# Kernel tuning notes

Hardware: AMD Instinct MI355X
Metric: run time of the kernel (lower is better)

Reference implementation:

```python
import jax, jax.numpy as jnp
import numpy as np

N, E, G = 100000, 3200000, 5000
EPS = 1e-5
HEADS, HC = 8, 16


def setup_inputs() -> dict:
    key = jax.random.key(0)
    k = jax.random.split(key, 12)

    def lin(kk, fi, fo):
        return (jax.random.normal(kk, (fi, fo), jnp.float32) / np.sqrt(fi)).astype(jnp.float32)

    return {
        "x": jax.random.normal(k[0], (N, 20), jnp.float32),
        "edge_index": jax.random.randint(k[1], (2, E), 0, N, dtype=jnp.int32),
        "batch": jnp.sort(jax.random.randint(k[2], (N,), 0, G, dtype=jnp.int32)),
        "W1": lin(k[3], 20, 64), "b1": jnp.zeros((64,), jnp.float32),
        "g1": jnp.ones((64,), jnp.float32), "be1": jnp.zeros((64,), jnp.float32),
        "W2": lin(k[4], 64, 32), "b2": jnp.zeros((32,), jnp.float32),
        "g2": jnp.ones((32,), jnp.float32), "be2": jnp.zeros((32,), jnp.float32),
        "W3": lin(k[5], 32, 16), "b3": jnp.zeros((16,), jnp.float32),
        "g3": jnp.ones((16,), jnp.float32), "be3": jnp.zeros((16,), jnp.float32),
        "Wg": lin(k[6], 16, HEADS * HC),
        "att_src": jax.random.normal(k[7], (HEADS, HC), jnp.float32) * 0.1,
        "att_dst": jax.random.normal(k[8], (HEADS, HC), jnp.float32) * 0.1,
        "bg": jnp.zeros((HC,), jnp.float32),
        "Wf": lin(k[9], 16, 3), "bf": jnp.zeros((3,), jnp.float32),
    }


def reference(x, edge_index, batch,
              W1, b1, g1, be1, W2, b2, g2, be2, W3, b3, g3, be3,
              Wg, att_src, att_dst, bg, Wf, bf):
    src, dst = edge_index[0], edge_index[1]
    loop = jnp.arange(N, dtype=src.dtype)
    src_sl = jnp.concatenate([src, loop])  # self-loops (GCN + GAT add_self_loops)
    dst_sl = jnp.concatenate([dst, loop])

    # GCN symmetric normalization D^-1/2 (A+I) D^-1/2
    deg = jax.ops.segment_sum(jnp.ones_like(src_sl, dtype=jnp.float32), dst_sl, N)
    dinv = jnp.where(deg > 0, 1.0 / jnp.sqrt(deg), 0.0)
    norm = (dinv[src_sl] * dinv[dst_sl])[:, None]  # [E+N, 1]

    def gcn(h, W, b):
        h = h @ W
        return jax.ops.segment_sum(h[src_sl] * norm, dst_sl, N) + b

    def bn_relu(h, g, b):  # BatchNorm1d (train-mode batch stats) + ReLU
        mu = h.mean(0)
        var = ((h - mu) ** 2).mean(0)
        return jax.nn.relu(g * (h - mu) * jax.lax.rsqrt(var + EPS) + b)

    h = bn_relu(gcn(x, W1, b1), g1, be1)   # dropout = identity (eval)
    h = bn_relu(gcn(h, W2, b2), g2, be2)
    h = bn_relu(gcn(h, W3, b3), g3, be3)

    # GATConv: heads=8, concat=False (mean over heads), eval -> no dropout
    xg = (h @ Wg).reshape(N, HEADS, HC)
    a_src = (xg * att_src).sum(-1)  # [N, H]
    a_dst = (xg * att_dst).sum(-1)
    logit = jax.nn.leaky_relu(a_src[src_sl] + a_dst[dst_sl], 0.2)  # [E+N, H]
    m = jax.ops.segment_max(logit, dst_sl, N)          # segment softmax over dst
    e = jnp.exp(logit - m[dst_sl])
    s = jax.ops.segment_sum(e, dst_sl, N)
    alpha = e / s[dst_sl]
    agg = jax.ops.segment_sum(xg[src_sl] * alpha[:, :, None], dst_sl, N)  # [N,H,C]
    hg = agg.mean(1) + bg  # [N, 16]

    pooled = jax.ops.segment_sum(hg, batch, G)  # global_add_pool -> [G, 16]
    return pooled @ Wf + bf  # [G, 3]
```

## Files before the change

kernel.cpp:

```cpp
#include <hip/hip_runtime.h>
#include <hip/hip_fp16.h>

constexpr int NN = 100000;
constexpr int EE = 3200000;
constexpr int GG = 5000;
constexpr float BNEPS = 1e-5f;

constexpr int BINS = 128;
constexpr int NPB = (NN + BINS - 1) / BINS;
constexpr int BCHUNK = 8192;
constexpr int NBCH = (EE + BCHUNK - 1) / BCHUNK;
constexpr int BINCAP2 = 96;
constexpr int BINREG = 27648;
constexpr int LCAP = 26624;
constexpr int CTR_STRIDE = 32;

typedef int int4v __attribute__((ext_vector_type(4)));


__global__ __launch_bounds__(1024) void bin_edges(const int* __restrict__ ei,
                                                  uint2* __restrict__ pairs,
                                                  int* __restrict__ binCur) {
    __shared__ int bcnt[BINS];
    __shared__ int bbase[BINS];
    __shared__ uint2 buf[BINS][BINCAP2];
    const int t = threadIdx.x;
    const int lane = t & 63, wv = t >> 6;
    for (int ch = blockIdx.x; ch < NBCH; ch += gridDim.x) {
        for (int k = t; k < BINS; k += 1024) bcnt[k] = 0;
        __syncthreads();
        const int qbase = ch * (BCHUNK / 4);
#pragma unroll
        for (int rep = 0; rep < 2; ++rep) {
            const int q = qbase + rep * 1024 + t;
            if (q < EE / 4) {
                int4v d = __builtin_nontemporal_load((const int4v*)(ei + EE) + q);
                int4v s = __builtin_nontemporal_load((const int4v*)ei + q);
                int dd[4] = {d.x, d.y, d.z, d.w};
                int ss[4] = {s.x, s.y, s.z, s.w};
#pragma unroll
                for (int k = 0; k < 4; ++k) {
                    int o = dd[k] / NPB;
                    int p = atomicAdd(&bcnt[o], 1);
                    if (p < BINCAP2) {
                        buf[o][p] = make_uint2((unsigned)dd[k], (unsigned)ss[k]);
                    } else {
                        int gp = atomicAdd(&binCur[o * CTR_STRIDE], 1);
                        pairs[(size_t)o * BINREG + gp] =
                            make_uint2((unsigned)dd[k], (unsigned)ss[k]);
                    }
                }
            }
        }
        __syncthreads();
        if (t < BINS) {
            int c = bcnt[t] < BINCAP2 ? bcnt[t] : BINCAP2;
            bbase[t] = atomicAdd(&binCur[t * CTR_STRIDE], c);
            bcnt[t] = c;
        }
        __syncthreads();
        for (int o = wv; o < BINS; o += 16) {
            const int c = bcnt[o];
            const size_t base = (size_t)o * BINREG + bbase[o];
            for (int k = lane; k < c; k += 64) pairs[base + k] = buf[o][k];
        }
        __syncthreads();
    }
}


__global__ void bin_base(const int* __restrict__ binCur, int* __restrict__ binBase) {
    __shared__ int s[BINS];
    const int t = threadIdx.x;
    const int v = binCur[t * CTR_STRIDE];
    s[t] = v;
    __syncthreads();
    for (int off = 1; off < BINS; off <<= 1) {
        int add = (t >= off) ? s[t - off] : 0;
        __syncthreads();
        s[t] += add;
        __syncthreads();
    }
    binBase[t] = s[t] - v;
}


__global__ __launch_bounds__(1024) void scatter_lds(const uint2* __restrict__ pairs,
                                                    const int* __restrict__ binCur,
                                                    const int* __restrict__ binBase,
                                                    int* __restrict__ rowptr,
                                                    float* __restrict__ dinv,
                                                    int* __restrict__ colA) {
    __shared__ int scnt[NPB];
    __shared__ int sscan[1024];
    __shared__ int lbuf[LCAP];
    const int b = blockIdx.x;
    const int t = threadIdx.x;
    const int lo = b * NPB;
    const int hi = (lo + NPB < NN) ? lo + NPB : NN;
    const int nb = hi - lo;
    const int tot = binCur[b * CTR_STRIDE];
    const int base = binBase[b];
    const uint2* p = pairs + (size_t)b * BINREG;
    for (int k = t; k < nb; k += 1024) scnt[k] = 0;
    __syncthreads();
    for (int q = t; q < tot; q += 1024) atomicAdd(&scnt[p[q].x - lo], 1);
    __syncthreads();
    const int myc = (t < nb) ? scnt[t] : 0;
    sscan[t] = myc;
    __syncthreads();
    for (int off = 1; off < 1024; off <<= 1) {
        int add = (t >= off) ? sscan[t - off] : 0;
        __syncthreads();
        sscan[t] += add;
        __syncthreads();
    }
    const int excl = sscan[t] - myc;
    if (t < nb) {
        rowptr[lo + t] = base + excl;
        dinv[lo + t] = rsqrtf((float)(myc + 1));
        scnt[t] = excl;
    }
    if (b == BINS - 1 && t == 0) rowptr[NN] = base + tot;
    __syncthreads();
    for (int q = t; q < tot; q += 1024) {
        uint2 e = p[q];
        int pos = atomicAdd(&scnt[e.x - lo], 1);
        if (pos < LCAP) lbuf[pos] = (int)e.y;
        else colA[base + pos] = (int)e.y;
    }
    __syncthreads();
    const int m = tot < LCAP ? tot : LCAP;
    for (int k = t; k < m; k += 1024) colA[base + k] = lbuf[k];
}


__global__ void scale_x(const float* __restrict__ x, const float* __restrict__ dinv,
                        __half* __restrict__ xsc) {
    int idx = blockIdx.x * blockDim.x + threadIdx.x;
    if (idx < NN * 20) {
        int n = idx / 20;
        xsc[idx] = __float2half(x[idx] * dinv[n]);
    }
}


template <int FIN, int FOUT, bool AFFINE, bool SCALED, bool STATS>
__global__ void gemm_k(const float* __restrict__ hin,
                       const float* __restrict__ sumsIn, const float* __restrict__ ssqIn,
                       const float* __restrict__ g, const float* __restrict__ be,
                       const float* __restrict__ W, const float* __restrict__ dinv,
                       const float* __restrict__ bias,
                       float* __restrict__ outF, __half* __restrict__ outH,
                       float* __restrict__ sumsOut, float* __restrict__ ssqOut) {
    constexpr int NB = 256 / FOUT;
    __shared__ float Wl[FIN * FOUT];
    __shared__ float rows[NB][FIN];
    __shared__ float aa[AFFINE ? FIN : 1], bb[AFFINE ? FIN : 1];
    const int t = threadIdx.x;
    if constexpr (AFFINE) {
        if (t < FIN) {
            float mu = sumsIn[t] / (float)NN;
            float var = ssqIn[t] / (float)NN - mu * mu;
            float a = g[t] * rsqrtf(var + BNEPS);
            aa[t] = a;
            bb[t] = be[t] - mu * a;
        }
    }
    for (int i = t; i < FIN * FOUT; i += 256) Wl[i] = W[i];
    const int c = t % FOUT, s = t / FOUT;
    const int ngrp = (NN + NB - 1) / NB;
    float sAcc = 0.f, qAcc = 0.f;
    for (int grp = blockIdx.x; grp < ngrp; grp += gridDim.x) {
        __syncthreads();
        for (int i = t; i < NB * FIN; i += 256) {
            int sn = i / FIN, k = i % FIN;
            int n2 = grp * NB + sn;
            float v = 0.f;
            if (n2 < NN) {
                v = hin[(size_t)n2 * FIN + k];
                if constexpr (AFFINE) {
                    v = aa[k] * v + bb[k];
                    v = v > 0.f ? v : 0.f;
                }
            }
            rows[sn][k] = v;
        }
        __syncthreads();
        int node = grp * NB + s;
        if (node < NN) {
            float acc = 0.f;
#pragma unroll
            for (int k = 0; k < FIN; ++k) acc += rows[s][k] * Wl[k * FOUT + c];
            if constexpr (SCALED) {
                outH[(size_t)node * FOUT + c] = __float2half(acc * dinv[node]);
            } else {
                float val = acc + bias[c];
                outF[(size_t)node * FOUT + c] = val;
                if constexpr (STATS) { sAcc += val; qAcc += val * val; }
            }
        }
    }
    if constexpr (STATS) {
        __shared__ float ls[FOUT], lq[FOUT];
        __syncthreads();
        if (t < FOUT) { ls[t] = 0.f; lq[t] = 0.f; }
        __syncthreads();
        atomicAdd(&ls[c], sAcc);
        atomicAdd(&lq[c], qAcc);
        __syncthreads();
        if (t < FOUT) { atomicAdd(&sumsOut[t], ls[t]); atomicAdd(&ssqOut[t], lq[t]); }
    }
}


template <int H2, int OUTF, bool STATS>
__global__ void agg_half(const __half2* __restrict__ src, const int* __restrict__ rowptr,
                         const int* __restrict__ colA, const float* __restrict__ dinv,
                         const float* __restrict__ bias, float* __restrict__ out,
                         float* __restrict__ sumsOut, float* __restrict__ ssqOut) {
    constexpr int SUB = 64 / H2;
    const int lane = threadIdx.x & 63;
    const int wid = (blockIdx.x * blockDim.x + threadIdx.x) >> 6;
    const int totalWaves = (gridDim.x * blockDim.x) >> 6;
    const int f = lane % H2;
    const int sub = lane / H2;
    const int stride = totalWaves * SUB;
    float bx = 0.f, by = 0.f;
    if (bias != nullptr) {
        bx = bias[2 * f];
        by = (2 * f + 1 < OUTF) ? bias[2 * f + 1] : 0.f;
    }
    const int i0 = (sub < SUB) ? wid * SUB + sub : NN;
    float sx = 0.f, qx = 0.f, sy = 0.f, qy = 0.f;
    for (int i = i0; i < NN; i += stride) {
        const int r0 = rowptr[i], r1 = rowptr[i + 1];
        float2 acc = __half22float2(src[(size_t)i * H2 + f]);
        float2 acc2 = {0.f, 0.f};
        int e = r0;
        for (; e + 3 < r1; e += 4) {
            int j0 = colA[e], j1 = colA[e + 1], j2 = colA[e + 2], j3 = colA[e + 3];
            float2 v0 = __half22float2(src[(size_t)j0 * H2 + f]);
            float2 v1 = __half22float2(src[(size_t)j1 * H2 + f]);
            float2 v2 = __half22float2(src[(size_t)j2 * H2 + f]);
            float2 v3 = __half22float2(src[(size_t)j3 * H2 + f]);
            acc.x += v0.x + v1.x;
            acc.y += v0.y + v1.y;
            acc2.x += v2.x + v3.x;
            acc2.y += v2.y + v3.y;
        }
        for (; e < r1; ++e) {
            float2 v = __half22float2(src[(size_t)colA[e] * H2 + f]);
            acc.x += v.x; acc.y += v.y;
        }
        acc.x += acc2.x; acc.y += acc2.y;
        const float d = dinv[i];
        float vx = d * acc.x + bx;
        out[(size_t)i * OUTF + 2 * f] = vx;
        if constexpr (STATS) { sx += vx; qx += vx * vx; }
        if (2 * f + 1 < OUTF) {
            float vy = d * acc.y + by;
            out[(size_t)i * OUTF + 2 * f + 1] = vy;
            if constexpr (STATS) { sy += vy; qy += vy * vy; }
        }
    }
    if constexpr (STATS) {
        __shared__ float ls[OUTF], lq[OUTF];
        const int t = threadIdx.x;
        if (t < OUTF) { ls[t] = 0.f; lq[t] = 0.f; }
        __syncthreads();
        atomicAdd(&ls[2 * f], sx);
        atomicAdd(&lq[2 * f], qx);
        if (2 * f + 1 < OUTF) {
            atomicAdd(&ls[2 * f + 1], sy);
            atomicAdd(&lq[2 * f + 1], qy);
        }
        __syncthreads();
        if (t < OUTF) { atomicAdd(&sumsOut[t], ls[t]); atomicAdd(&ssqOut[t], lq[t]); }
    }
}


__global__ void gat_mats(const float* __restrict__ Wg, const float* __restrict__ att_src,
                         const float* __restrict__ att_dst, const float* __restrict__ Wf,
                         const float* __restrict__ bg, float* __restrict__ Psrc,
                         float* __restrict__ Pdst, float* __restrict__ M,
                         float* __restrict__ bgW) {
    int t = threadIdx.x;
    if (t < 128) {
        int k = t >> 3, h = t & 7;
        float s = 0.f, d = 0.f;
        for (int c = 0; c < 16; ++c) {
            float wv = Wg[k * 128 + h * 16 + c];
            s += wv * att_src[h * 16 + c];
            d += wv * att_dst[h * 16 + c];
        }
        Psrc[k * 8 + h] = s;
        Pdst[k * 8 + h] = d;
    } else if (t < 512) {
        int m = t - 128;
        if (m < 384) {
            int hk = m / 3, j = m - hk * 3;
            int H = hk >> 4, k = hk & 15;
            float s = 0.f;
            for (int c = 0; c < 16; ++c) s += Wg[k * 128 + H * 16 + c] * Wf[c * 3 + j];
            M[hk * 3 + j] = 0.125f * s;
        }
    } else if (t < 515) {
        int j = t - 512;
        float s = 0.f;
        for (int c = 0; c < 16; ++c) s += bg[c] * Wf[c * 3 + j];
        bgW[j] = s;
    }
}


__global__ void gat_pre2(const float* __restrict__ h3,
                         const float* __restrict__ sums3, const float* __restrict__ ssq3,
                         const float* __restrict__ g3, const float* __restrict__ be3,
                         const float* __restrict__ Psrc, const float* __restrict__ Pdst,
                         float4* __restrict__ zas, float* __restrict__ adst) {
    __shared__ float Ps[128], Pd[128], aa[16], bb[16];
    int t = threadIdx.x;
    if (t < 128) { Ps[t] = Psrc[t]; Pd[t] = Pdst[t]; }
    if (t < 16) {
        float mu = sums3[t] / (float)NN;
        float var = ssq3[t] / (float)NN - mu * mu;
        float a = g3[t] * rsqrtf(var + BNEPS);
        aa[t] = a;
        bb[t] = be3[t] - mu * a;
    }
    __syncthreads();
    int n = blockIdx.x * blockDim.x + t;
    if (n >= NN) return;
    float zv[16];
#pragma unroll
    for (int k = 0; k < 16; ++k) {
        float v = h3[(size_t)n * 16 + k];
        v = aa[k] * v + bb[k];
        zv[k] = v > 0.f ? v : 0.f;
    }
    __half2 zh[8];
#pragma unroll
    for (int k = 0; k < 8; ++k) zh[k] = __floats2half2_rn(zv[2 * k], zv[2 * k + 1]);
    float as[8], ad[8];
#pragma unroll
    for (int h = 0; h < 8; ++h) { as[h] = 0.f; ad[h] = 0.f; }
#pragma unroll
    for (int k = 0; k < 16; ++k) {
        float zk = zv[k];
#pragma unroll
        for (int h = 0; h < 8; ++h) {
            as[h] += zk * Ps[k * 8 + h];
            ad[h] += zk * Pd[k * 8 + h];
        }
    }
    float4* zrow = zas + (size_t)n * 4;
    zrow[0] = ((float4*)zh)[0];
    zrow[1] = ((float4*)zh)[1];
    zrow[2] = make_float4(as[0], as[1], as[2], as[3]);
    zrow[3] = make_float4(as[4], as[5], as[6], as[7]);
    float4* d4 = (float4*)(adst + (size_t)n * 8);
    d4[0] = make_float4(ad[0], ad[1], ad[2], ad[3]);
    d4[1] = make_float4(ad[4], ad[5], ad[6], ad[7]);
}


__device__ __forceinline__ float leaky02(float x) { return x > 0.f ? x : 0.2f * x; }

__global__ void gat_agg7(const float4* __restrict__ zas, const float* __restrict__ adst,
                         const int* __restrict__ rowptr, const int* __restrict__ colA,
                         const int* __restrict__ batch, const float* __restrict__ Mg,
                         float* __restrict__ out) {
    __shared__ float Ml[384];
    for (int k = threadIdx.x; k < 384; k += 256) Ml[k] = Mg[k];
    __syncthreads();
    const int lane = threadIdx.x & 63;
    const int ls = lane & 7;
    const int q = ls & 3;
    const int hh = ls >> 2;
    const int grp = lane >> 3;
    const int gb = lane & 56;
    const int wid = (blockIdx.x * blockDim.x + threadIdx.x) >> 6;
    const int totalWaves = (gridDim.x * blockDim.x) >> 6;
    const int stride = totalWaves * 8;
    const char* zb = (const char*)zas;
    for (int i = wid * 8 + grp; i < NN; i += stride) {
        const int r0 = rowptr[i], r1 = rowptr[i + 1];
        const float adv = __builtin_nontemporal_load(adst + (size_t)i * 8 + ls);
        float acc[4][4];
        float wsum[4];
#pragma unroll
        for (int h = 0; h < 4; ++h) {
            wsum[h] = 0.f;
#pragma unroll
            for (int k = 0; k < 4; ++k) acc[h][k] = 0.f;
        }
        auto compute = [&](float av, float2 zr, bool val) {
            const __half2* zp = (const __half2*)&zr;
            const float2 f0 = __half22float2(zp[0]), f1 = __half22float2(zp[1]);
            const float zf[4] = {f0.x, f0.y, f1.x, f1.y};
            const float w = val ? __expf(leaky02(av + adv)) : 0.f;
            float wq[4];
#pragma unroll
            for (int h = 0; h < 4; ++h) wq[h] = __shfl(w, gb + hh * 4 + h);
#pragma unroll
            for (int h = 0; h < 4; ++h) {
                wsum[h] += wq[h];
#pragma unroll
                for (int k = 0; k < 4; ++k) acc[h][k] += wq[h] * zf[k];
            }
        };
        int e = r0;
        int jA = i, jB = i;
        bool vB = false;
        if (e < r1) { jB = colA[e]; ++e; vB = true; }
        const char* rowA = zb + (size_t)jA * 64;
        const char* rowB = zb + (size_t)jB * 64;
        float avA = *(const float*)(rowA + 32 + ls * 4);
        float2 zA = *(const float2*)(rowA + q * 8);
        float avB = *(const float*)(rowB + 32 + ls * 4);
        float2 zB = *(const float2*)(rowB + q * 8);
        while (true) {
            int jA2 = i, jB2 = i;
            bool vA2 = false, vB2 = false;
            if (e < r1) { jA2 = colA[e]; ++e; vA2 = true; }
            if (e < r1) { jB2 = colA[e]; ++e; vB2 = true; }
            const char* rA2 = zb + (size_t)jA2 * 64;
            const char* rB2 = zb + (size_t)jB2 * 64;
            float avA2 = *(const float*)(rA2 + 32 + ls * 4);
            float2 zA2 = *(const float2*)(rA2 + q * 8);
            float avB2 = *(const float*)(rB2 + 32 + ls * 4);
            float2 zB2 = *(const float2*)(rB2 + q * 8);
            compute(avA, zA, true);
            compute(avB, zB, vB);
            if (!vA2) break;
            avA = avA2; zA = zA2; avB = avB2; zB = zB2; vB = vB2;
        }
        float o0 = 0.f, o1 = 0.f, o2 = 0.f;
#pragma unroll
        for (int h = 0; h < 4; ++h) {
            const float inv = 1.f / wsum[h];
            const int hk0 = (hh * 4 + h) * 16 + q * 4;
#pragma unroll
            for (int k = 0; k < 4; ++k) {
                const float v = acc[h][k] * inv;
                const float* m = &Ml[(hk0 + k) * 3];
                o0 += v * m[0];
                o1 += v * m[1];
                o2 += v * m[2];
            }
        }
#pragma unroll
        for (int off = 1; off < 8; off <<= 1) {
            o0 += __shfl_xor(o0, off);
            o1 += __shfl_xor(o1, off);
            o2 += __shfl_xor(o2, off);
        }
        const int g = batch[i];
        if (ls < 3) {
            const float ov = (ls == 0) ? o0 : (ls == 1) ? o1 : o2;
            atomicAdd(&out[g * 3 + ls], ov);
        }
    }
}


__global__ void graph_bounds(const int* __restrict__ batch, int* __restrict__ gstart) {
    int n = blockIdx.x * blockDim.x + threadIdx.x;
    if (n < NN) {
        int bn = batch[n];
        int bp = (n == 0) ? -1 : batch[n - 1];
        for (int g = bp + 1; g <= bn; ++g) gstart[g] = n;
        if (n == NN - 1)
            for (int g = bn + 1; g <= GG; ++g) gstart[g] = NN;
    }
}


__global__ void pool_init(const int* __restrict__ gstart, const float* __restrict__ bgW,
                          const float* __restrict__ bf, float* __restrict__ out) {
    int g = blockIdx.x * blockDim.x + threadIdx.x;
    if (g < GG) {
        float cnt = (float)(gstart[g + 1] - gstart[g]);
#pragma unroll
        for (int j = 0; j < 3; ++j) out[g * 3 + j] = cnt * bgW[j] + bf[j];
    }
}


extern "C" void kernel_launch(void* const* d_in, const int* in_sizes, int n_in,
                              void* d_out, int out_size, void* d_ws, size_t ws_size,
                              hipStream_t stream) {
    const float* x = (const float*)d_in[0];
    const int* ei = (const int*)d_in[1];
    const int* batch = (const int*)d_in[2];
    const float* W1 = (const float*)d_in[3];  const float* b1 = (const float*)d_in[4];
    const float* g1 = (const float*)d_in[5];  const float* be1 = (const float*)d_in[6];
    const float* W2 = (const float*)d_in[7];  const float* b2 = (const float*)d_in[8];
    const float* g2 = (const float*)d_in[9];  const float* be2 = (const float*)d_in[10];
    const float* W3 = (const float*)d_in[11]; const float* b3 = (const float*)d_in[12];
    const float* g3 = (const float*)d_in[13]; const float* be3 = (const float*)d_in[14];
    const float* Wg = (const float*)d_in[15];
    const float* att_src = (const float*)d_in[16];
    const float* att_dst = (const float*)d_in[17];
    const float* bg = (const float*)d_in[18];
    const float* Wf = (const float*)d_in[19];
    const float* bf = (const float*)d_in[20];
    float* out = (float*)d_out;

    char* w = (char*)d_ws;
    auto alloc = [&](size_t bytes) -> char* {
        char* p = w;
        w += (bytes + 255) & ~(size_t)255;
        return p;
    };
    int* binCur = (int*)alloc((size_t)BINS * CTR_STRIDE * 4);
    float* sums1 = (float*)alloc(64 * 4); float* ssq1 = (float*)alloc(64 * 4);
    float* sums2 = (float*)alloc(32 * 4); float* ssq2 = (float*)alloc(32 * 4);
    float* sums3 = (float*)alloc(16 * 4); float* ssq3 = (float*)alloc(16 * 4);
    size_t zeroBytes = (size_t)(w - (char*)d_ws);
    int* binBase = (int*)alloc((size_t)BINS * 4);
    float* Psrc = (float*)alloc(128 * 4);
    float* Pdst = (float*)alloc(128 * 4);
    float* Mm = (float*)alloc(384 * 4);
    float* bgW = (float*)alloc(3 * 4);
    int* gstart = (int*)alloc((size_t)(GG + 1) * 4);
    int* rowptr = (int*)alloc((size_t)(NN + 1) * 4);
    int* colA = (int*)alloc((size_t)EE * 4);
    float* dinv = (float*)alloc((size_t)NN * 4);
    char* A = alloc((size_t)NN * 64 * 4);
    char* B = alloc((size_t)NN * 64 * 4);

    uint2*  pairs = (uint2*)A;
    __half* xsc  = (__half*)B;
    float*  aggx = (float*)(B + (size_t)NN * 32 * 2);
    float*  h1   = (float*)A;
    __half* hs2  = (__half*)B;
    float*  h2   = (float*)(B + (size_t)NN * 32 * 2);
    __half* hs3  = (__half*)A;
    float*  h3   = (float*)(A + (size_t)NN * 16 * 2);
    char*   zas  = A + (size_t)NN * 96;
    float*  adst = (float*)(A + (size_t)NN * 160);

    hipMemsetAsync(d_ws, 0, zeroBytes, stream);

    bin_edges<<<256, 1024, 0, stream>>>(ei, pairs, binCur);
    bin_base<<<1, BINS, 0, stream>>>(binCur, binBase);
    scatter_lds<<<BINS, 1024, 0, stream>>>(pairs, binCur, binBase, rowptr, dinv, colA);
    gat_mats<<<1, 1024, 0, stream>>>(Wg, att_src, att_dst, Wf, bg, Psrc, Pdst, Mm, bgW);
    graph_bounds<<<(NN + 255) / 256, 256, 0, stream>>>(batch, gstart);
    pool_init<<<(GG + 255) / 256, 256, 0, stream>>>(gstart, bgW, bf, out);

    scale_x<<<(NN * 20 + 255) / 256, 256, 0, stream>>>(x, dinv, xsc);
    agg_half<10, 20, false><<<2048, 256, 0, stream>>>((const __half2*)xsc, rowptr, colA, dinv,
                                                      nullptr, aggx, nullptr, nullptr);
    gemm_k<20, 64, false, false, true><<<2048, 256, 0, stream>>>(
        aggx, nullptr, nullptr, nullptr, nullptr, W1, dinv, b1, h1, nullptr, sums1, ssq1);

    gemm_k<64, 32, true, true, false><<<2048, 256, 0, stream>>>(
        h1, sums1, ssq1, g1, be1, W2, dinv, nullptr, nullptr, hs2, nullptr, nullptr);
    agg_half<16, 32, true><<<2048, 256, 0, stream>>>((const __half2*)hs2, rowptr, colA, dinv,
                                                     b2, h2, sums2, ssq2);

    gemm_k<32, 16, true, true, false><<<2048, 256, 0, stream>>>(
        h2, sums2, ssq2, g2, be2, W3, dinv, nullptr, nullptr, hs3, nullptr, nullptr);
    agg_half<8, 16, true><<<2048, 256, 0, stream>>>((const __half2*)hs3, rowptr, colA, dinv,
                                                    b3, h3, sums3, ssq3);

    gat_pre2<<<(NN + 255) / 256, 256, 0, stream>>>(h3, sums3, ssq3, g3, be3, Psrc, Pdst,
                                                   (float4*)zas, adst);
    gat_agg7<<<3200, 256, 0, stream>>>((const float4*)zas, adst, rowptr, colA, batch, Mm, out);
}
```

Before: 468.9 us.

## Pack edge pairs into 32-bit words, store intermediates in fp16, split layer-2 aggregation

Edge binning now packs each edge's local destination offset and source index into one 32-bit word instead of a uint2, halving the traffic through the pairs buffer. All intermediate activations (aggx, h1, h2, h3) are stored as fp16 instead of fp32, cutting the bytes each layer reads and writes. The 32-wide layer-2 aggregation is split into two 16-wide feature halves with separate buffers, and the next GEMM reads both halves. The risks are lower precision in the pre-BatchNorm activations, although the statistics are still accumulated in fp32, and an extra pass over the CSR graph for layer 2.

```diff
diff --git a/kernel.cpp b/kernel.cpp
--- a/kernel.cpp
+++ b/kernel.cpp
@@ -18,12 +18,13 @@
 typedef int int4v __attribute__((ext_vector_type(4)));
 
 
+
 __global__ __launch_bounds__(1024) void bin_edges(const int* __restrict__ ei,
-                                                  uint2* __restrict__ pairs,
+                                                  unsigned* __restrict__ pairs,
                                                   int* __restrict__ binCur) {
     __shared__ int bcnt[BINS];
     __shared__ int bbase[BINS];
-    __shared__ uint2 buf[BINS][BINCAP2];
+    __shared__ unsigned buf[BINS][BINCAP2];
     const int t = threadIdx.x;
     const int lane = t & 63, wv = t >> 6;
     for (int ch = blockIdx.x; ch < NBCH; ch += gridDim.x) {
@@ -41,13 +42,13 @@
 #pragma unroll
                 for (int k = 0; k < 4; ++k) {
                     int o = dd[k] / NPB;
+                    unsigned pk = ((unsigned)(dd[k] - o * NPB) << 17) | (unsigned)ss[k];
                     int p = atomicAdd(&bcnt[o], 1);
                     if (p < BINCAP2) {
-                        buf[o][p] = make_uint2((unsigned)dd[k], (unsigned)ss[k]);
+                        buf[o][p] = pk;
                     } else {
                         int gp = atomicAdd(&binCur[o * CTR_STRIDE], 1);
-                        pairs[(size_t)o * BINREG + gp] =
-                            make_uint2((unsigned)dd[k], (unsigned)ss[k]);
+                        pairs[(size_t)o * BINREG + gp] = pk;
                     }
                 }
             }
@@ -85,7 +86,7 @@
 }
 
 
-__global__ __launch_bounds__(1024) void scatter_lds(const uint2* __restrict__ pairs,
+__global__ __launch_bounds__(1024) void scatter_lds(const unsigned* __restrict__ pairs,
                                                     const int* __restrict__ binCur,
                                                     const int* __restrict__ binBase,
                                                     int* __restrict__ rowptr,
@@ -101,10 +102,10 @@
     const int nb = hi - lo;
     const int tot = binCur[b * CTR_STRIDE];
     const int base = binBase[b];
-    const uint2* p = pairs + (size_t)b * BINREG;
+    const unsigned* p = pairs + (size_t)b * BINREG;
     for (int k = t; k < nb; k += 1024) scnt[k] = 0;
     __syncthreads();
-    for (int q = t; q < tot; q += 1024) atomicAdd(&scnt[p[q].x - lo], 1);
+    for (int q = t; q < tot; q += 1024) atomicAdd(&scnt[p[q] >> 17], 1);
     __syncthreads();
     const int myc = (t < nb) ? scnt[t] : 0;
     sscan[t] = myc;
@@ -124,10 +125,11 @@
     if (b == BINS - 1 && t == 0) rowptr[NN] = base + tot;
     __syncthreads();
     for (int q = t; q < tot; q += 1024) {
-        uint2 e = p[q];
-        int pos = atomicAdd(&scnt[e.x - lo], 1);
-        if (pos < LCAP) lbuf[pos] = (int)e.y;
-        else colA[base + pos] = (int)e.y;
+        unsigned e = p[q];
+        int pos = atomicAdd(&scnt[e >> 17], 1);
+        int src = (int)(e & 0x1FFFFu);
+        if (pos < LCAP) lbuf[pos] = src;
+        else colA[base + pos] = src;
     }
     __syncthreads();
     const int m = tot < LCAP ? tot : LCAP;
@@ -145,13 +147,13 @@
 }
 
 
-template <int FIN, int FOUT, bool AFFINE, bool SCALED, bool STATS>
-__global__ void gemm_k(const float* __restrict__ hin,
+template <int FIN, int FOUT, bool AFFINE, bool SCALED, bool STATS, bool DUAL, bool SPLITOUT>
+__global__ void gemm_k(const __half* __restrict__ hinA, const __half* __restrict__ hinB,
                        const float* __restrict__ sumsIn, const float* __restrict__ ssqIn,
                        const float* __restrict__ g, const float* __restrict__ be,
                        const float* __restrict__ W, const float* __restrict__ dinv,
                        const float* __restrict__ bias,
-                       float* __restrict__ outF, __half* __restrict__ outH,
+                       __half* __restrict__ outA, __half* __restrict__ outB,
                        float* __restrict__ sumsOut, float* __restrict__ ssqOut) {
     constexpr int NB = 256 / FOUT;
     __shared__ float Wl[FIN * FOUT];
@@ -178,7 +180,14 @@
             int n2 = grp * NB + sn;
             float v = 0.f;
             if (n2 < NN) {
-                v = hin[(size_t)n2 * FIN + k];
+                __half hv;
+                if constexpr (DUAL) {
+                    hv = (k < FIN / 2) ? hinA[(size_t)n2 * (FIN / 2) + k]
+                                       : hinB[(size_t)n2 * (FIN / 2) + k - FIN / 2];
+                } else {
+                    hv = hinA[(size_t)n2 * FIN + k];
+                }
+                v = __half2float(hv);
                 if constexpr (AFFINE) {
                     v = aa[k] * v + bb[k];
                     v = v > 0.f ? v : 0.f;
@@ -193,10 +202,15 @@
 #pragma unroll
             for (int k = 0; k < FIN; ++k) acc += rows[s][k] * Wl[k * FOUT + c];
             if constexpr (SCALED) {
-                outH[(size_t)node * FOUT + c] = __float2half(acc * dinv[node]);
+                __half hv = __float2half(acc * dinv[node]);
+                if constexpr (SPLITOUT) {
+                    ((c < FOUT / 2) ? outA : outB)[(size_t)node * (FOUT / 2) + (c % (FOUT / 2))] = hv;
+                } else {
+                    outA[(size_t)node * FOUT + c] = hv;
+                }
             } else {
                 float val = acc + bias[c];
-                outF[(size_t)node * FOUT + c] = val;
+                outA[(size_t)node * FOUT + c] = __float2half(val);
                 if constexpr (STATS) { sAcc += val; qAcc += val * val; }
             }
         }
@@ -217,7 +231,7 @@
 template <int H2, int OUTF, bool STATS>
 __global__ void agg_half(const __half2* __restrict__ src, const int* __restrict__ rowptr,
                          const int* __restrict__ colA, const float* __restrict__ dinv,
-                         const float* __restrict__ bias, float* __restrict__ out,
+                         const float* __restrict__ bias, __half* __restrict__ out,
                          float* __restrict__ sumsOut, float* __restrict__ ssqOut) {
     constexpr int SUB = 64 / H2;
     const int lane = threadIdx.x & 63;
@@ -229,7 +243,7 @@
     float bx = 0.f, by = 0.f;
     if (bias != nullptr) {
         bx = bias[2 * f];
-        by = (2 * f + 1 < OUTF) ? bias[2 * f + 1] : 0.f;
+        by = bias[2 * f + 1];
     }
     const int i0 = (sub < SUB) ? wid * SUB + sub : NN;
     float sx = 0.f, qx = 0.f, sy = 0.f, qy = 0.f;
@@ -256,13 +270,9 @@
         acc.x += acc2.x; acc.y += acc2.y;
         const float d = dinv[i];
         float vx = d * acc.x + bx;
-        out[(size_t)i * OUTF + 2 * f] = vx;
-        if constexpr (STATS) { sx += vx; qx += vx * vx; }
-        if (2 * f + 1 < OUTF) {
-            float vy = d * acc.y + by;
-            out[(size_t)i * OUTF + 2 * f + 1] = vy;
-            if constexpr (STATS) { sy += vy; qy += vy * vy; }
-        }
+        float vy = d * acc.y + by;
+        *(__half2*)(out + (size_t)i * OUTF + 2 * f) = __floats2half2_rn(vx, vy);
+        if constexpr (STATS) { sx += vx; qx += vx * vx; sy += vy; qy += vy * vy; }
     }
     if constexpr (STATS) {
         __shared__ float ls[OUTF], lq[OUTF];
@@ -271,10 +281,8 @@
         __syncthreads();
         atomicAdd(&ls[2 * f], sx);
         atomicAdd(&lq[2 * f], qx);
-        if (2 * f + 1 < OUTF) {
-            atomicAdd(&ls[2 * f + 1], sy);
-            atomicAdd(&lq[2 * f + 1], qy);
-        }
+        atomicAdd(&ls[2 * f + 1], sy);
+        atomicAdd(&lq[2 * f + 1], qy);
         __syncthreads();
         if (t < OUTF) { atomicAdd(&sumsOut[t], ls[t]); atomicAdd(&ssqOut[t], lq[t]); }
     }
@@ -315,7 +323,7 @@
 }
 
 
-__global__ void gat_pre2(const float* __restrict__ h3,
+__global__ void gat_pre2(const __half* __restrict__ h3,
                          const float* __restrict__ sums3, const float* __restrict__ ssq3,
                          const float* __restrict__ g3, const float* __restrict__ be3,
                          const float* __restrict__ Psrc, const float* __restrict__ Pdst,
@@ -333,12 +341,18 @@
     __syncthreads();
     int n = blockIdx.x * blockDim.x + t;
     if (n >= NN) return;
+    union { float4 f4[2]; __half2 h2v[8]; } u;
+    const float4* hp = (const float4*)(h3 + (size_t)n * 16);
+    u.f4[0] = hp[0];
+    u.f4[1] = hp[1];
     float zv[16];
 #pragma unroll
-    for (int k = 0; k < 16; ++k) {
-        float v = h3[(size_t)n * 16 + k];
-        v = aa[k] * v + bb[k];
-        zv[k] = v > 0.f ? v : 0.f;
+    for (int k = 0; k < 8; ++k) {
+        float2 p = __half22float2(u.h2v[k]);
+        float v0 = aa[2 * k] * p.x + bb[2 * k];
+        float v1 = aa[2 * k + 1] * p.y + bb[2 * k + 1];
+        zv[2 * k] = v0 > 0.f ? v0 : 0.f;
+        zv[2 * k + 1] = v1 > 0.f ? v1 : 0.f;
     }
     __half2 zh[8];
 #pragma unroll
@@ -532,14 +546,16 @@
     char* A = alloc((size_t)NN * 64 * 4);
     char* B = alloc((size_t)NN * 64 * 4);
 
-    uint2*  pairs = (uint2*)A;
+    unsigned* pairs = (unsigned*)A;
     __half* xsc  = (__half*)B;
-    float*  aggx = (float*)(B + (size_t)NN * 32 * 2);
-    float*  h1   = (float*)A;
-    __half* hs2  = (__half*)B;
-    float*  h2   = (float*)(B + (size_t)NN * 32 * 2);
+    __half* aggx = (__half*)(B + (size_t)NN * 64);
+    __half* h1   = (__half*)A;
+    __half* hs2a = (__half*)B;
+    __half* hs2b = (__half*)(B + (size_t)NN * 32);
+    __half* h2a  = (__half*)(B + (size_t)NN * 64);
+    __half* h2b  = (__half*)(B + (size_t)NN * 96);
     __half* hs3  = (__half*)A;
-    float*  h3   = (float*)(A + (size_t)NN * 16 * 2);
+    __half* h3   = (__half*)(A + (size_t)NN * 32);
     char*   zas  = A + (size_t)NN * 96;
     float*  adst = (float*)(A + (size_t)NN * 160);
 
@@ -555,16 +571,19 @@
     scale_x<<<(NN * 20 + 255) / 256, 256, 0, stream>>>(x, dinv, xsc);
     agg_half<10, 20, false><<<2048, 256, 0, stream>>>((const __half2*)xsc, rowptr, colA, dinv,
                                                       nullptr, aggx, nullptr, nullptr);
-    gemm_k<20, 64, false, false, true><<<2048, 256, 0, stream>>>(
-        aggx, nullptr, nullptr, nullptr, nullptr, W1, dinv, b1, h1, nullptr, sums1, ssq1);
-
-    gemm_k<64, 32, true, true, false><<<2048, 256, 0, stream>>>(
-        h1, sums1, ssq1, g1, be1, W2, dinv, nullptr, nullptr, hs2, nullptr, nullptr);
-    agg_half<16, 32, true><<<2048, 256, 0, stream>>>((const __half2*)hs2, rowptr, colA, dinv,
-                                                     b2, h2, sums2, ssq2);
-
-    gemm_k<32, 16, true, true, false><<<2048, 256, 0, stream>>>(
-        h2, sums2, ssq2, g2, be2, W3, dinv, nullptr, nullptr, hs3, nullptr, nullptr);
+    gemm_k<20, 64, false, false, true, false, false><<<2048, 256, 0, stream>>>(
+        aggx, nullptr, nullptr, nullptr, nullptr, nullptr, W1, dinv, b1, h1, nullptr,
+        sums1, ssq1);
+
+    gemm_k<64, 32, true, true, false, false, true><<<2048, 256, 0, stream>>>(
+        h1, nullptr, sums1, ssq1, g1, be1, W2, dinv, nullptr, hs2a, hs2b, nullptr, nullptr);
+    agg_half<8, 16, true><<<2048, 256, 0, stream>>>((const __half2*)hs2a, rowptr, colA, dinv,
+                                                    b2, h2a, sums2, ssq2);
+    agg_half<8, 16, true><<<2048, 256, 0, stream>>>((const __half2*)hs2b, rowptr, colA, dinv,
+                                                    b2 + 16, h2b, sums2 + 16, ssq2 + 16);
+
+    gemm_k<32, 16, true, true, false, true, false><<<2048, 256, 0, stream>>>(
+        h2a, h2b, sums2, ssq2, g2, be2, W3, dinv, nullptr, hs3, nullptr, nullptr, nullptr);
     agg_half<8, 16, true><<<2048, 256, 0, stream>>>((const __half2*)hs3, rowptr, colA, dinv,
                                                     b3, h3, sums3, ssq3);
 
```

New measurement: 493.8 us. 5.3% more time.
